# Kernel optimization log

Measured on AMD Instinct MI355X. Metric: run time of the kernel, lower is better.

Reference implementation:

```python
import jax, jax.numpy as jnp
import numpy as np

INPUT_DIM = 512
HIDDEN_DIM = 512


def _linear_params(key, in_dim, out_dim):
    kw, kb = jax.random.split(key)
    bound = 1.0 / np.sqrt(in_dim)
    W = jax.random.uniform(kw, (out_dim, in_dim), minval=-bound, maxval=bound, dtype=jnp.float32)
    b = jax.random.uniform(kb, (out_dim,), minval=-bound, maxval=bound, dtype=jnp.float32)
    return W, b


def setup_inputs() -> dict:
    key = jax.random.key(0)
    keys = jax.random.split(key, 11)
    B = 8192
    inp = {
        "x_t": jax.random.normal(keys[0], (B, INPUT_DIM), dtype=jnp.float32),
        "h_tm1": jax.random.normal(keys[1], (B, HIDDEN_DIM), dtype=jnp.float32),
        "c_tm1": jax.random.normal(keys[2], (B, HIDDEN_DIM), dtype=jnp.float32),
    }
    names = ["f_x", "f_h", "i_x", "i_h", "g_x", "g_h", "o_x", "o_h"]
    for n, k in zip(names, keys[3:]):
        in_dim = INPUT_DIM if n.endswith("_x") else HIDDEN_DIM
        W, b = _linear_params(k, in_dim, HIDDEN_DIM)
        inp[f"W_{n}"] = W
        inp[f"b_{n}"] = b
    return inp


def reference(x_t, h_tm1, c_tm1,
              W_f_x, b_f_x, W_f_h, b_f_h,
              W_i_x, b_i_x, W_i_h, b_i_h,
              W_g_x, b_g_x, W_g_h, b_g_h,
              W_o_x, b_o_x, W_o_h, b_o_h):
    # Stacked weights: [4, H, D] -> einsum over D gives [B, 4, H].
    Wx = jnp.stack([W_f_x, W_g_x, W_i_x, W_o_x])  # [4, H, Din]
    bx = jnp.stack([b_f_x, b_g_x, b_i_x, b_o_x])  # [4, H]
    Wh = jnp.stack([W_f_h, W_g_h, W_i_h, W_o_h])
    bh = jnp.stack([b_f_h, b_g_h, b_i_h, b_o_h])
    pre = (jnp.einsum('bd,ghd->bgh', x_t, Wx) + bx
           + jnp.einsum('bd,ghd->bgh', h_tm1, Wh) + bh)  # [B, 4, H]
    f_t = jax.nn.sigmoid(pre[:, 0])
    g_t = jnp.tanh(pre[:, 1])
    i_t = jax.nn.sigmoid(pre[:, 2])
    o_t = jax.nn.sigmoid(pre[:, 3])
    c_t = f_t * c_tm1 + i_t * g_t
    h_t = o_t * jnp.tanh(c_t)
    return (h_t, c_t)
```

## Files before the change

### kernel.cpp

```cpp
#include <hip/hip_runtime.h>
#include <cstdint>
#include <cstddef>


typedef __attribute__((ext_vector_type(8))) short short8;
typedef __attribute__((ext_vector_type(4))) float floatx4;

#define AS1(p) ((const __attribute__((address_space(1))) void*)(p))
#define AS3(p) ((__attribute__((address_space(3))) void*)(p))

__device__ __forceinline__ unsigned short f2bf(float f) {
  union { float f; unsigned u; } v; v.f = f;
  unsigned u = v.u;
  return (unsigned short)((u + 0x7fffu + ((u >> 16) & 1u)) >> 16);
}

struct PackArgs {
  const float* x; const float* h;
  const float* wx[4]; const float* wh[4];
  const float* bx[4]; const float* bh[4];
  unsigned short* A; unsigned short* B; float* bias;
};

__global__ __launch_bounds__(256) void pack_all_kernel(PackArgs P) {
  const int bid = blockIdx.x;
  if (bid < 8192) {
    int e = (bid * 256 + threadIdx.x) * 4;
    int b = e >> 10, k = e & 1023;
    const float* src = (k < 512) ? (P.x + b * 512 + k)
                                 : (P.h + b * 512 + (k - 512));
    float4 v = *(const float4*)src;
    ushort4 o;
    o.x = f2bf(v.x); o.y = f2bf(v.y); o.z = f2bf(v.z); o.w = f2bf(v.w);
    *(ushort4*)(P.A + e) = o;
  } else {
    int e = ((bid - 8192) * 256 + threadIdx.x) * 4;
    int n = e >> 10, k = e & 1023;
    int g = n >> 9, hh = n & 511;
    const float* src = (k < 512) ? (P.wx[g] + hh * 512 + k)
                                 : (P.wh[g] + hh * 512 + (k - 512));
    float4 v = *(const float4*)src;
    ushort4 o;
    o.x = f2bf(v.x); o.y = f2bf(v.y); o.z = f2bf(v.z); o.w = f2bf(v.w);
    *(ushort4*)(P.B + e) = o;
    if (k == 0) P.bias[n] = P.bx[g][hh] + P.bh[g][hh];
  }
}

__global__ __launch_bounds__(512, 4)
void lstm_gemm_kernel(const unsigned short* __restrict__ A,
                      const unsigned short* __restrict__ B,
                      const float* __restrict__ bias,
                      const float* __restrict__ c_prev,
                      float* __restrict__ h_out,
                      float* __restrict__ c_out) {
  __shared__ __align__(16) char smem[49152];
  __shared__ float biasS[128];

  const int tid  = threadIdx.x;
  const int lane = tid & 63;
  const int w    = tid >> 6;
  const int quad = lane >> 4;
  const int colA = lane & 15;
  const int m0   = blockIdx.x * 256;
  const int h0   = blockIdx.y * 32;

  if (tid < 128) {
    biasS[tid] = bias[(tid >> 5) * 512 + h0 + (tid & 31)];
  }

  const int srow = tid >> 3;
  const int cl   = tid & 7;
  const int cg   = cl ^ (srow & 7);

  floatx4 acc[4][4];
#pragma unroll
  for (int i = 0; i < 4; ++i)
#pragma unroll
    for (int j = 0; j < 4; ++j) acc[i][j] = (floatx4){0.f, 0.f, 0.f, 0.f};

  const int wm = (w >> 1) * 64;
  const int wn = (w & 1) * 64;

  const char* Ag = (const char*)A;
  const char* Bg = (const char*)B;

  for (int kt = 0; kt < 16; ++kt) {
    __syncthreads();
    const int kb = kt * 128;
#pragma unroll
    for (int j = 0; j < 4; ++j) {
      int r = j * 64 + srow;
      __builtin_amdgcn_global_load_lds(
          AS1(Ag + (size_t)(m0 + r) * 2048 + kb + cg * 16),
          AS3(smem + r * 128 + cl * 16), 16, 0, 0);
    }
#pragma unroll
    for (int j = 0; j < 2; ++j) {
      int r = j * 64 + srow;
      int grow = (r >> 5) * 512 + h0 + (r & 31);
      __builtin_amdgcn_global_load_lds(
          AS1(Bg + (size_t)grow * 2048 + kb + cg * 16),
          AS3(smem + 32768 + r * 128 + cl * 16), 16, 0, 0);
    }
    __syncthreads();

#pragma unroll
    for (int kk = 0; kk < 2; ++kk) {
      const int off = ((kk * 4 + quad) ^ (colA & 7)) * 16;
      short8 af[4], bfr[4];
#pragma unroll
      for (int mi = 0; mi < 4; ++mi)
        af[mi] = *(const short8*)(smem + (wm + mi * 16 + colA) * 128 + off);
#pragma unroll
      for (int ni = 0; ni < 4; ++ni)
        bfr[ni] = *(const short8*)(smem + 32768 + (wn + ni * 16 + colA) * 128 + off);
#pragma unroll
      for (int mi = 0; mi < 4; ++mi)
#pragma unroll
        for (int ni = 0; ni < 4; ++ni)
          acc[mi][ni] = __builtin_amdgcn_mfma_f32_16x16x32_bf16(
              af[mi], bfr[ni], acc[mi][ni], 0, 0, 0);
    }
  }

  __syncthreads();
  float* ep = (float*)smem;
#pragma unroll
  for (int rd = 0; rd < 4; ++rd) {
    if ((w >> 1) == rd) {
#pragma unroll
      for (int mi = 0; mi < 4; ++mi)
#pragma unroll
        for (int ni = 0; ni < 4; ++ni) {
          int rr0 = mi * 16 + quad * 4;
          int cc  = wn + ni * 16 + colA;
#pragma unroll
          for (int rr = 0; rr < 4; ++rr)
            ep[(rr0 + rr) * 132 + cc] = acc[mi][ni][rr];
        }
    }
    __syncthreads();
#pragma unroll
    for (int j = 0; j < 4; ++j) {
      int idx  = j * 512 + tid;
      int mloc = idx >> 5;
      int hh   = idx & 31;
      float pf = ep[mloc * 132 +      hh] + biasS[hh];
      float pi = ep[mloc * 132 + 32 + hh] + biasS[32 + hh];
      float pg = ep[mloc * 132 + 64 + hh] + biasS[64 + hh];
      float po = ep[mloc * 132 + 96 + hh] + biasS[96 + hh];
      float fg = 1.f / (1.f + __expf(-pf));
      float ig = 1.f / (1.f + __expf(-pi));
      float gg = 1.f - 2.f / (1.f + __expf(2.f * pg));
      float og = 1.f / (1.f + __expf(-po));
      int m  = m0 + rd * 64 + mloc;
      int hg = h0 + hh;
      float cp = c_prev[m * 512 + hg];
      float cv = fg * cp + ig * gg;
      float th = 1.f - 2.f / (1.f + __expf(2.f * cv));
      h_out[m * 512 + hg] = og * th;
      c_out[m * 512 + hg] = cv;
    }
    __syncthreads();
  }
}

extern "C" void kernel_launch(void* const* d_in, const int* in_sizes, int n_in,
                              void* d_out, int out_size, void* d_ws, size_t ws_size,
                              hipStream_t stream) {
  char* ws = (char*)d_ws;
  unsigned short* Abf = (unsigned short*)ws;
  unsigned short* Bbf = (unsigned short*)(ws + (size_t)16777216);
  float* bias = (float*)(ws + (size_t)16777216 + 4194304);

  float* hout = (float*)d_out;
  float* cout = hout + (size_t)8192 * 512;

  PackArgs P;
  P.x = (const float*)d_in[0];
  P.h = (const float*)d_in[1];
  P.wx[0] = (const float*)d_in[3];  P.bx[0] = (const float*)d_in[4];
  P.wh[0] = (const float*)d_in[5];  P.bh[0] = (const float*)d_in[6];
  P.wx[1] = (const float*)d_in[7];  P.bx[1] = (const float*)d_in[8];
  P.wh[1] = (const float*)d_in[9];  P.bh[1] = (const float*)d_in[10];
  P.wx[2] = (const float*)d_in[11]; P.bx[2] = (const float*)d_in[12];
  P.wh[2] = (const float*)d_in[13]; P.bh[2] = (const float*)d_in[14];
  P.wx[3] = (const float*)d_in[15]; P.bx[3] = (const float*)d_in[16];
  P.wh[3] = (const float*)d_in[17]; P.bh[3] = (const float*)d_in[18];
  P.A = Abf; P.B = Bbf; P.bias = bias;

  pack_all_kernel<<<10240, 256, 0, stream>>>(P);

  const float* c = (const float*)d_in[2];
  dim3 grid(32, 16);
  lstm_gemm_kernel<<<grid, 512, 0, stream>>>(Abf, Bbf, bias, c, hout, cout);
}
```

Measured before the change: 170.5 us.

## Enlarge GEMM tile to 256x256 with double-buffered async LDS pipeline

The GEMM tile grows from 256x128 to 256x256 output columns, covering 64 hidden units across all four gates, and each wave now holds an 8x4 MFMA accumulator block. Global-to-LDS loads are split into half-K stages and double-buffered, with explicit vmcnt/lgkmcnt waits, barriers and s_setprio, so loads for the next tiles overlap MFMA work. The intent is to raise arithmetic intensity and hide memory latency. In exchange it uses 128KB of LDS and more registers, cuts occupancy to 2 blocks per CU, and halves the grid to 256 blocks.

```diff
diff --git a/kernel.cpp b/kernel.cpp
--- a/kernel.cpp
+++ b/kernel.cpp
@@ -47,15 +47,32 @@
   }
 }
 
-__global__ __launch_bounds__(512, 4)
+
+#define LDS4(dst, BASEOFF) do {                                   \
+    dst[0] = *(const short8*)(smem + (BASEOFF));                  \
+    dst[1] = *(const short8*)(smem + (BASEOFF) + 1024);           \
+    dst[2] = *(const short8*)(smem + (BASEOFF) + 2048);           \
+    dst[3] = *(const short8*)(smem + (BASEOFF) + 3072);           \
+  } while (0)
+
+#define MFMA16(MB) do {                                           \
+    _Pragma("unroll")                                             \
+    for (int i_ = 0; i_ < 4; ++i_)                                \
+      _Pragma("unroll")                                           \
+      for (int j_ = 0; j_ < 4; ++j_)                              \
+        acc[(MB) + i_][j_] = __builtin_amdgcn_mfma_f32_16x16x32_bf16( \
+            af[i_], bf[j_], acc[(MB) + i_][j_], 0, 0, 0);         \
+  } while (0)
+
+__global__ __launch_bounds__(512, 2)
 void lstm_gemm_kernel(const unsigned short* __restrict__ A,
                       const unsigned short* __restrict__ B,
                       const float* __restrict__ bias,
                       const float* __restrict__ c_prev,
                       float* __restrict__ h_out,
                       float* __restrict__ c_out) {
-  __shared__ __align__(16) char smem[49152];
-  __shared__ float biasS[128];
+  __shared__ __align__(16) char smem[131072];
+  __shared__ float biasS[256];
 
   const int tid  = threadIdx.x;
   const int lane = tid & 63;
@@ -63,93 +80,140 @@
   const int quad = lane >> 4;
   const int colA = lane & 15;
   const int m0   = blockIdx.x * 256;
-  const int h0   = blockIdx.y * 32;
-
-  if (tid < 128) {
-    biasS[tid] = bias[(tid >> 5) * 512 + h0 + (tid & 31)];
-  }
-
-  const int srow = tid >> 3;
-  const int cl   = tid & 7;
-  const int cg   = cl ^ (srow & 7);
-
-  floatx4 acc[4][4];
-#pragma unroll
-  for (int i = 0; i < 4; ++i)
-#pragma unroll
-    for (int j = 0; j < 4; ++j) acc[i][j] = (floatx4){0.f, 0.f, 0.f, 0.f};
-
-  const int wm = (w >> 1) * 64;
-  const int wn = (w & 1) * 64;
+  const int h0   = blockIdx.y * 64;
+
+  if (tid < 256) {
+    biasS[tid] = bias[(tid >> 6) * 512 + h0 + (tid & 63)];
+  }
+
+  const int wm = (w >> 2) * 128;
+  const int wn = (w & 3) * 64;
+
+  const int swzR = (quad ^ ((colA >> 1) & 3)) * 16;
+  const int rdA  = (wm + colA) * 64 + swzR;
+  const int rdB  = (wn + colA) * 64 + swzR;
+
+  const int lrow   = lane >> 2;
+  const int swzS   = ((lane & 3) ^ ((lane >> 3) & 3)) * 16;
+  const int sgArow = m0 + w * 32 + lrow;
+  const int growB0 = ((2 * w + 0) >> 2) * 512 + h0 + ((w * 32) & 63) + lrow;
+  const int growB1 = ((2 * w + 1) >> 2) * 512 + h0 + ((w * 32 + 16) & 63) + lrow;
+  const int ldsStage = w * 2048 + lane * 16;
 
   const char* Ag = (const char*)A;
   const char* Bg = (const char*)B;
 
+  floatx4 acc[8][4];
+#pragma unroll
+  for (int i = 0; i < 8; ++i)
+#pragma unroll
+    for (int j = 0; j < 4; ++j) acc[i][j] = (floatx4){0.f, 0.f, 0.f, 0.f};
+
+  auto stageA = [&](int ktt, int kh, int bb) {
+    const int kb = (ktt & 15) * 128 + kh * 64;
+#pragma unroll
+    for (int l = 0; l < 2; ++l)
+      __builtin_amdgcn_global_load_lds(
+          AS1(Ag + (size_t)(sgArow + l * 16) * 2048 + kb + swzS),
+          AS3(smem + bb * 32768 + kh * 16384 + ldsStage + l * 1024), 16, 0, 0);
+  };
+  auto stageB = [&](int ktt, int kh, int bb) {
+    const int kb = (ktt & 15) * 128 + kh * 64;
+    __builtin_amdgcn_global_load_lds(
+        AS1(Bg + (size_t)growB0 * 2048 + kb + swzS),
+        AS3(smem + 65536 + bb * 32768 + kh * 16384 + ldsStage), 16, 0, 0);
+    __builtin_amdgcn_global_load_lds(
+        AS1(Bg + (size_t)growB1 * 2048 + kb + swzS),
+        AS3(smem + 65536 + bb * 32768 + kh * 16384 + ldsStage + 1024), 16, 0, 0);
+  };
+
+  stageA(0, 0, 0); stageB(0, 0, 0);
+  stageA(0, 1, 0); stageB(0, 1, 0);
+  stageA(1, 0, 1); stageB(1, 0, 1);
+  asm volatile("s_waitcnt vmcnt(8)" ::: "memory");
+  __builtin_amdgcn_s_barrier();
+  asm volatile("" ::: "memory");
+
+  short8 af[4], bf[4];
+
   for (int kt = 0; kt < 16; ++kt) {
-    __syncthreads();
-    const int kb = kt * 128;
-#pragma unroll
-    for (int j = 0; j < 4; ++j) {
-      int r = j * 64 + srow;
-      __builtin_amdgcn_global_load_lds(
-          AS1(Ag + (size_t)(m0 + r) * 2048 + kb + cg * 16),
-          AS3(smem + r * 128 + cl * 16), 16, 0, 0);
-    }
-#pragma unroll
-    for (int j = 0; j < 2; ++j) {
-      int r = j * 64 + srow;
-      int grow = (r >> 5) * 512 + h0 + (r & 31);
-      __builtin_amdgcn_global_load_lds(
-          AS1(Bg + (size_t)grow * 2048 + kb + cg * 16),
-          AS3(smem + 32768 + r * 128 + cl * 16), 16, 0, 0);
-    }
-    __syncthreads();
-
-#pragma unroll
-    for (int kk = 0; kk < 2; ++kk) {
-      const int off = ((kk * 4 + quad) ^ (colA & 7)) * 16;
-      short8 af[4], bfr[4];
-#pragma unroll
-      for (int mi = 0; mi < 4; ++mi)
-        af[mi] = *(const short8*)(smem + (wm + mi * 16 + colA) * 128 + off);
-#pragma unroll
-      for (int ni = 0; ni < 4; ++ni)
-        bfr[ni] = *(const short8*)(smem + 32768 + (wn + ni * 16 + colA) * 128 + off);
-#pragma unroll
-      for (int mi = 0; mi < 4; ++mi)
-#pragma unroll
-        for (int ni = 0; ni < 4; ++ni)
-          acc[mi][ni] = __builtin_amdgcn_mfma_f32_16x16x32_bf16(
-              af[mi], bfr[ni], acc[mi][ni], 0, 0, 0);
-    }
-  }
-
+    const int buf = kt & 1;
+    const int bA  = buf * 32768;
+    const int bB  = 65536 + buf * 32768;
+
+    LDS4(af, bA + rdA);
+    LDS4(bf, bB + rdB);
+    stageA(kt + 1, 1, buf ^ 1);
+    __builtin_amdgcn_s_barrier();
+    asm volatile("s_waitcnt lgkmcnt(0)" ::: "memory");
+    __builtin_amdgcn_s_setprio(1);
+    MFMA16(0);
+    __builtin_amdgcn_s_setprio(0);
+    __builtin_amdgcn_s_barrier();
+
+    LDS4(af, bA + rdA + 4096);
+    stageB(kt + 1, 1, buf ^ 1);
+    __builtin_amdgcn_s_barrier();
+    asm volatile("s_waitcnt lgkmcnt(0)" ::: "memory");
+    __builtin_amdgcn_s_setprio(1);
+    MFMA16(4);
+    __builtin_amdgcn_s_setprio(0);
+    asm volatile("s_waitcnt vmcnt(8)" ::: "memory");
+    __builtin_amdgcn_s_barrier();
+    asm volatile("" ::: "memory");
+
+    LDS4(af, bA + 16384 + rdA);
+    LDS4(bf, bB + 16384 + rdB);
+    stageA(kt + 2, 0, buf);
+    __builtin_amdgcn_s_barrier();
+    asm volatile("s_waitcnt lgkmcnt(0)" ::: "memory");
+    __builtin_amdgcn_s_setprio(1);
+    MFMA16(0);
+    __builtin_amdgcn_s_setprio(0);
+    __builtin_amdgcn_s_barrier();
+
+    LDS4(af, bA + 16384 + rdA + 4096);
+    stageB(kt + 2, 0, buf);
+    __builtin_amdgcn_s_barrier();
+    asm volatile("s_waitcnt lgkmcnt(0)" ::: "memory");
+    __builtin_amdgcn_s_setprio(1);
+    MFMA16(4);
+    __builtin_amdgcn_s_setprio(0);
+    asm volatile("s_waitcnt vmcnt(8)" ::: "memory");
+    __builtin_amdgcn_s_barrier();
+    asm volatile("" ::: "memory");
+  }
+
+  asm volatile("s_waitcnt vmcnt(0)" ::: "memory");
   __syncthreads();
+
   float* ep = (float*)smem;
+  const int gate = w & 3;
 #pragma unroll
   for (int rd = 0; rd < 4; ++rd) {
-    if ((w >> 1) == rd) {
-#pragma unroll
-      for (int mi = 0; mi < 4; ++mi)
+    if ((w >> 2) == (rd >> 1)) {
+      const int mib = (rd & 1) * 4;
+#pragma unroll
+      for (int mi2 = 0; mi2 < 4; ++mi2)
 #pragma unroll
         for (int ni = 0; ni < 4; ++ni) {
-          int rr0 = mi * 16 + quad * 4;
-          int cc  = wn + ni * 16 + colA;
+          int rr0 = mi2 * 16 + quad * 4;
+          int cc  = gate * 64 + ni * 16 + colA;
 #pragma unroll
           for (int rr = 0; rr < 4; ++rr)
-            ep[(rr0 + rr) * 132 + cc] = acc[mi][ni][rr];
+            ep[(rr0 + rr) * 258 + cc] = acc[mib + mi2][ni][rr];
         }
     }
     __syncthreads();
 #pragma unroll
-    for (int j = 0; j < 4; ++j) {
+    for (int j = 0; j < 8; ++j) {
       int idx  = j * 512 + tid;
-      int mloc = idx >> 5;
-      int hh   = idx & 31;
-      float pf = ep[mloc * 132 +      hh] + biasS[hh];
-      float pi = ep[mloc * 132 + 32 + hh] + biasS[32 + hh];
-      float pg = ep[mloc * 132 + 64 + hh] + biasS[64 + hh];
-      float po = ep[mloc * 132 + 96 + hh] + biasS[96 + hh];
+      int mloc = idx >> 6;
+      int hh   = idx & 63;
+      float pf = ep[mloc * 258 +       hh] + biasS[hh];
+      float pi = ep[mloc * 258 +  64 + hh] + biasS[64 + hh];
+      float pg = ep[mloc * 258 + 128 + hh] + biasS[128 + hh];
+      float po = ep[mloc * 258 + 192 + hh] + biasS[192 + hh];
       float fg = 1.f / (1.f + __expf(-pf));
       float ig = 1.f / (1.f + __expf(-pi));
       float gg = 1.f - 2.f / (1.f + __expf(2.f * pg));
@@ -193,6 +257,6 @@
   pack_all_kernel<<<10240, 256, 0, stream>>>(P);
 
   const float* c = (const float*)d_in[2];
-  dim3 grid(32, 16);
+  dim3 grid(32, 8);
   lstm_gemm_kernel<<<grid, 512, 0, stream>>>(Abf, Bbf, bias, c, hout, cout);
 }
```

Result: slower. 178.4 us (+4.7%).

## Interleave gate weights, shrink GEMM tile to 128x128, and prefetch c_prev in epilogue

Applied to the files above, without the earlier changes.

The packed weight matrix is reordered so the four gates of each hidden unit sit in adjacent rows, which lets B-tile loads be contiguous and the epilogue read all four gate preactivations and biases as one float4. The GEMM block shrinks from 256x128 with 512 threads to 128x128 with 256 threads, doubling the grid and cutting LDS per block, which is meant to improve occupancy and wave balance across CUs. c_prev values are loaded into registers before the epilogue barrier so their global latency overlaps the accumulator spill to LDS. The trade-off is lower A-tile reuse per block and more register pressure in the epilogue.

```diff
diff --git a/kernel.cpp b/kernel.cpp
--- a/kernel.cpp
+++ b/kernel.cpp
@@ -36,7 +36,7 @@
   } else {
     int e = ((bid - 8192) * 256 + threadIdx.x) * 4;
     int n = e >> 10, k = e & 1023;
-    int g = n >> 9, hh = n & 511;
+    int g = n & 3, hh = n >> 2;
     const float* src = (k < 512) ? (P.wx[g] + hh * 512 + k)
                                  : (P.wh[g] + hh * 512 + (k - 512));
     float4 v = *(const float4*)src;
@@ -47,27 +47,29 @@
   }
 }
 
-__global__ __launch_bounds__(512, 4)
+__global__ __launch_bounds__(256, 4)
 void lstm_gemm_kernel(const unsigned short* __restrict__ A,
                       const unsigned short* __restrict__ B,
                       const float* __restrict__ bias,
                       const float* __restrict__ c_prev,
                       float* __restrict__ h_out,
                       float* __restrict__ c_out) {
-  __shared__ __align__(16) char smem[49152];
-  __shared__ float biasS[128];
+  __shared__ __align__(16) char smem[33792];
+  __shared__ __align__(16) float biasS[128];
 
   const int tid  = threadIdx.x;
   const int lane = tid & 63;
   const int w    = tid >> 6;
   const int quad = lane >> 4;
   const int colA = lane & 15;
-  const int m0   = blockIdx.x * 256;
+  const int m0   = blockIdx.x * 128;
+  const int n0   = blockIdx.y * 128;
   const int h0   = blockIdx.y * 32;
 
-  if (tid < 128) {
-    biasS[tid] = bias[(tid >> 5) * 512 + h0 + (tid & 31)];
-  }
+  if (tid < 128) biasS[tid] = bias[n0 + tid];
+
+  const int wm = (w >> 1) * 64;
+  const int wn = (w & 1) * 64;
 
   const int srow = tid >> 3;
   const int cl   = tid & 7;
@@ -79,9 +81,6 @@
 #pragma unroll
     for (int j = 0; j < 4; ++j) acc[i][j] = (floatx4){0.f, 0.f, 0.f, 0.f};
 
-  const int wm = (w >> 1) * 64;
-  const int wn = (w & 1) * 64;
-
   const char* Ag = (const char*)A;
   const char* Bg = (const char*)B;
 
@@ -90,18 +89,17 @@
     const int kb = kt * 128;
 #pragma unroll
     for (int j = 0; j < 4; ++j) {
-      int r = j * 64 + srow;
+      int r = j * 32 + srow;
       __builtin_amdgcn_global_load_lds(
           AS1(Ag + (size_t)(m0 + r) * 2048 + kb + cg * 16),
           AS3(smem + r * 128 + cl * 16), 16, 0, 0);
     }
 #pragma unroll
-    for (int j = 0; j < 2; ++j) {
-      int r = j * 64 + srow;
-      int grow = (r >> 5) * 512 + h0 + (r & 31);
+    for (int j = 0; j < 4; ++j) {
+      int r = j * 32 + srow;
       __builtin_amdgcn_global_load_lds(
-          AS1(Bg + (size_t)grow * 2048 + kb + cg * 16),
-          AS3(smem + 32768 + r * 128 + cl * 16), 16, 0, 0);
+          AS1(Bg + (size_t)(n0 + r) * 2048 + kb + cg * 16),
+          AS3(smem + 16384 + r * 128 + cl * 16), 16, 0, 0);
     }
     __syncthreads();
 
@@ -114,7 +112,7 @@
         af[mi] = *(const short8*)(smem + (wm + mi * 16 + colA) * 128 + off);
 #pragma unroll
       for (int ni = 0; ni < 4; ++ni)
-        bfr[ni] = *(const short8*)(smem + 32768 + (wn + ni * 16 + colA) * 128 + off);
+        bfr[ni] = *(const short8*)(smem + 16384 + (wn + ni * 16 + colA) * 128 + off);
 #pragma unroll
       for (int mi = 0; mi < 4; ++mi)
 #pragma unroll
@@ -127,7 +125,15 @@
   __syncthreads();
   float* ep = (float*)smem;
 #pragma unroll
-  for (int rd = 0; rd < 4; ++rd) {
+  for (int rd = 0; rd < 2; ++rd) {
+    float cp[8];
+#pragma unroll
+    for (int j = 0; j < 8; ++j) {
+      int idx  = j * 256 + tid;
+      int mloc = idx >> 5;
+      int hh   = idx & 31;
+      cp[j] = c_prev[(m0 + rd * 64 + mloc) * 512 + h0 + hh];
+    }
     if ((w >> 1) == rd) {
 #pragma unroll
       for (int mi = 0; mi < 4; ++mi)
@@ -142,23 +148,24 @@
     }
     __syncthreads();
 #pragma unroll
-    for (int j = 0; j < 4; ++j) {
-      int idx  = j * 512 + tid;
+    for (int j = 0; j < 8; ++j) {
+      int idx  = j * 256 + tid;
       int mloc = idx >> 5;
       int hh   = idx & 31;
-      float pf = ep[mloc * 132 +      hh] + biasS[hh];
-      float pi = ep[mloc * 132 + 32 + hh] + biasS[32 + hh];
-      float pg = ep[mloc * 132 + 64 + hh] + biasS[64 + hh];
-      float po = ep[mloc * 132 + 96 + hh] + biasS[96 + hh];
+      float4 pre = *(const float4*)(ep + mloc * 132 + hh * 4);
+      float4 bb  = *(const float4*)(biasS + hh * 4);
+      float pf = pre.x + bb.x;
+      float pi = pre.y + bb.y;
+      float pg = pre.z + bb.z;
+      float po = pre.w + bb.w;
       float fg = 1.f / (1.f + __expf(-pf));
       float ig = 1.f / (1.f + __expf(-pi));
       float gg = 1.f - 2.f / (1.f + __expf(2.f * pg));
       float og = 1.f / (1.f + __expf(-po));
+      float cv = fg * cp[j] + ig * gg;
+      float th = 1.f - 2.f / (1.f + __expf(2.f * cv));
       int m  = m0 + rd * 64 + mloc;
       int hg = h0 + hh;
-      float cp = c_prev[m * 512 + hg];
-      float cv = fg * cp + ig * gg;
-      float th = 1.f - 2.f / (1.f + __expf(2.f * cv));
       h_out[m * 512 + hg] = og * th;
       c_out[m * 512 + hg] = cv;
     }
@@ -193,6 +200,6 @@
   pack_all_kernel<<<10240, 256, 0, stream>>>(P);
 
   const float* c = (const float*)d_in[2];
-  dim3 grid(32, 16);
-  lstm_gemm_kernel<<<grid, 512, 0, stream>>>(Abf, Bbf, bias, c, hout, cout);
-}
+  dim3 grid(64, 16);
+  lstm_gemm_kernel<<<grid, 256, 0, stream>>>(Abf, Bbf, bias, c, hout, cout);
+}
```

Result: no change. 170.4 us (-0.1%).
